# Kernel optimization log

Measured on AMD Instinct MI355X. Metric: run time of the kernel, lower is better.

The kernel has to match this reference:

```python
import jax, jax.numpy as jnp
import numpy as np

V = 50000   # words_num
D = 128     # embedding_dim
B = 2048    # batch
P = 20      # max Huffman path length


def setup_inputs() -> dict:
    key = jax.random.key(0)
    k1, k2, k3, k4, k5 = jax.random.split(key, 5)
    inputs_vector = jax.random.uniform(k1, (B, V), dtype=jnp.float32)
    path_nodes_indices = jax.random.randint(k2, (B, P), 0, V)
    huffman_codes = jax.random.randint(k3, (B, P), 0, 2).astype(jnp.float32)
    mask = jnp.ones((B, P), dtype=jnp.float32)
    # learned params, torch nn.Linear weight layout [out, in], kaiming-uniform-ish scale
    W_emb = jax.random.uniform(k4, (D, V), dtype=jnp.float32, minval=-1.0, maxval=1.0) / np.sqrt(V)
    W_cls = jax.random.uniform(k5, (V, D), dtype=jnp.float32, minval=-1.0, maxval=1.0) / np.sqrt(D)
    return {
        "inputs_vector": inputs_vector,
        "W_emb": W_emb,
        "W_cls": W_cls,
        "path_nodes_indices": path_nodes_indices,
        "huffman_codes": huffman_codes,
        "mask": mask,
    }


def _bce_with_logits(logits, targets):
    # numerically stable, elementwise (reduction='none')
    return jnp.maximum(logits, 0.0) - logits * targets + jnp.log1p(jnp.exp(-jnp.abs(logits)))


def reference(inputs_vector, W_emb, W_cls, path_nodes_indices, huffman_codes, mask):
    x = inputs_vector @ W_emb.T              # [B, D]  embedding Linear (no bias)
    logits_full = x @ W_cls.T                # [B, V]  full-vocab cls matmul (as in source)
    logits = jnp.take_along_axis(logits_full, path_nodes_indices, axis=1)  # [B, P]
    loss = _bce_with_logits(logits, huffman_codes)  # [B, P]
    masked_loss = loss * mask
    per_sample = masked_loss.sum(axis=-1) / mask.sum(axis=-1)  # [B]
    return per_sample.mean()
```

## Files before the change

kernel.cpp:

```cpp
#include <hip/hip_runtime.h>
#include <hip/hip_bf16.h>

#define V 50000
#define D 128
#define B 2048
#define P 20

#define BM 128
#define BK 64
#define NSPLIT 48
#define KC 1056
#define VPAD (NSPLIT * KC)
#define NSLICE (VPAD / 32)
#define NMT (B / BM)

typedef float  f32x4  __attribute__((ext_vector_type(4)));
typedef short  bf16x8 __attribute__((ext_vector_type(8)));
typedef unsigned int uint4v __attribute__((ext_vector_type(4)));

__device__ __forceinline__ unsigned int pk2(float a, float b) {
    return (__float_as_uint(b) & 0xFFFF0000u) | (__float_as_uint(a) >> 16);
}
__device__ __forceinline__ unsigned short f2bf(float f) {
    unsigned int u = __float_as_uint(f);
    return (unsigned short)((u + 0x7FFFu + ((u >> 16) & 1u)) >> 16);
}
__device__ __forceinline__ bf16x8 pack8(f32x4 lo, f32x4 hi) {
    union { uint4v u; bf16x8 h; } r;
    r.u.x = pk2(lo[0], lo[1]); r.u.y = pk2(lo[2], lo[3]);
    r.u.z = pk2(hi[0], hi[1]); r.u.w = pk2(hi[2], hi[3]);
    return r.h;
}

__global__ __launch_bounds__(256)
void w2v_wcast(const float* __restrict__ Wemb, unsigned short* __restrict__ WTF) {
    __shared__ unsigned short L[128 * 128];
    const int bk = blockIdx.x;
    const int t  = threadIdx.x;
    const int d = t >> 1, h = t & 1;
    const float* src = Wemb + (size_t)d * V + bk * 128 + h * 64;
#pragma unroll
    for (int j = 0; j < 8; ++j) {
        const int kg = bk * 128 + h * 64 + j * 8;
        f32x4 v0 = {0,0,0,0}, v1 = {0,0,0,0};
        if (kg + 8 <= V) {
            const f32x4* p = reinterpret_cast<const f32x4*>(src + j * 8);
            v0 = p[0]; v1 = p[1];
        }
        uint4v u;
        u.x = pk2(v0[0], v0[1]); u.y = pk2(v0[2], v0[3]);
        u.z = pk2(v1[0], v1[1]); u.w = pk2(v1[2], v1[3]);
        const int c8 = h * 8 + j;
        *reinterpret_cast<uint4v*>((char*)L + d * 256 + ((c8 ^ (d & 15)) << 4)) = u;
    }
    __syncthreads();
    const int w = t >> 6, l = t & 63;
    const int kg4 = l >> 4, fr = l & 15;
#pragma unroll
    for (int sl = 0; sl < 4; ++sl)
#pragma unroll
        for (int j2 = 0; j2 < 2; ++j2) {
            const int n  = w + j2 * 4;
            const int dd = n * 16 + fr;
            const int c8 = sl * 4 + kg4;
            uint4v u = *reinterpret_cast<const uint4v*>(
                (char*)L + dd * 256 + ((c8 ^ (dd & 15)) << 4));
            *reinterpret_cast<uint4v*>(
                (char*)WTF + ((size_t)(bk * 4 + sl) * 8 + n) * 1024 + l * 16) = u;
        }
}

template<int FAST>
__global__ __launch_bounds__(256, 3)
void w2v_gemm(const float* __restrict__ Ain, const void* __restrict__ Wsrc,
              void* __restrict__ part) {
    __shared__ unsigned short Sm[2 * BM * BK];
    char* AsB = (char*)Sm;
    char* WsB = (char*)(Sm + BM * BK);

    const int i   = blockIdx.x;
    const int xcd = i & 7;
    const int q   = i >> 3;
    const int s   = xcd * 6 + (q >> 4);
    const int mt  = q & 15;
    const int m0  = mt * BM;
    const int k0  = s * KC;
    const int k1  = (k0 + KC < V) ? (k0 + KC) : V;
    const int nsteps = (k1 - k0 + 63) >> 6;

    const int tid  = threadIdx.x;
    const int lane = tid & 63;
    const int wid  = tid >> 6;
    const int w32  = wid * 32;
    const int fr   = lane & 15;
    const int kg4  = lane >> 4;

    f32x4 acc[2][8] = {};

    const int rbase = tid >> 3;
    const int c8    = tid & 7;
    const int c8x   = c8 ^ (rbase & 7);
    const float* aBase = Ain + (size_t)(m0 + rbase) * V + c8 * 8;
    const unsigned short* WT = (const unsigned short*)Wsrc;
    const float*          Wf = (const float*)Wsrc;

    f32x4 aR[8];
    uint4v wR[4];
    f32x4 wRf[8];

    auto loadregs = [&](int ks) {
        const bool ag = (ks + c8 * 8 + 8 <= k1);
#pragma unroll
        for (int it = 0; it < 4; ++it) {
            const float* ap = aBase + (size_t)(it * 32) * V + ks;
            if (ag) {
                aR[it * 2]     = *reinterpret_cast<const f32x4*>(ap);
                aR[it * 2 + 1] = *reinterpret_cast<const f32x4*>(ap + 4);
            } else {
                aR[it * 2] = f32x4{0.f, 0.f, 0.f, 0.f};
                aR[it * 2 + 1] = f32x4{0.f, 0.f, 0.f, 0.f};
            }
        }
        if (FAST) {
            const char* wb = (const char*)WT + (size_t)(ks >> 5) * 8192 + tid * 16;
#pragma unroll
            for (int it = 0; it < 4; ++it)
                wR[it] = *reinterpret_cast<const uint4v*>(wb + it * 4096);
        } else {
            const bool wg = (ks + c8 * 8 + 8 <= V);
#pragma unroll
            for (int it = 0; it < 4; ++it) {
                const float* wp = Wf + (size_t)(rbase + it * 32) * V + c8 * 8 + ks;
                if (wg) {
                    wRf[it * 2]     = *reinterpret_cast<const f32x4*>(wp);
                    wRf[it * 2 + 1] = *reinterpret_cast<const f32x4*>(wp + 4);
                } else {
                    wRf[it * 2] = f32x4{0.f, 0.f, 0.f, 0.f};
                    wRf[it * 2 + 1] = f32x4{0.f, 0.f, 0.f, 0.f};
                }
            }
        }
    };

    auto writeLDS = [&]() {
#pragma unroll
        for (int it = 0; it < 4; ++it) {
            const unsigned dstA = (unsigned)((rbase + it * 32) * 128) + (unsigned)(c8x * 16);
            uint4v ua;
            ua.x = pk2(aR[it * 2][0], aR[it * 2][1]);
            ua.y = pk2(aR[it * 2][2], aR[it * 2][3]);
            ua.z = pk2(aR[it * 2 + 1][0], aR[it * 2 + 1][1]);
            ua.w = pk2(aR[it * 2 + 1][2], aR[it * 2 + 1][3]);
            *reinterpret_cast<uint4v*>(AsB + dstA) = ua;
            if (FAST) {
                *reinterpret_cast<uint4v*>(WsB + tid * 16 + it * 4096) = wR[it];
            } else {
                const int d = rbase + it * 32;
                const unsigned dstW = (unsigned)(((c8 >> 2) * 8 + (d >> 4)) * 1024
                                     + ((c8 & 3) * 16 + (d & 15)) * 16);
                uint4v uw;
                uw.x = pk2(wRf[it * 2][0], wRf[it * 2][1]);
                uw.y = pk2(wRf[it * 2][2], wRf[it * 2][3]);
                uw.z = pk2(wRf[it * 2 + 1][0], wRf[it * 2 + 1][1]);
                uw.w = pk2(wRf[it * 2 + 1][2], wRf[it * 2 + 1][3]);
                *reinterpret_cast<uint4v*>(WsB + dstW) = uw;
            }
        }
    };

    loadregs(k0);

    for (int t = 0; t < nsteps; ++t) {
        writeLDS();
        asm volatile("s_waitcnt lgkmcnt(0)" ::: "memory");
        __builtin_amdgcn_s_barrier();
        if (t + 1 < nsteps) loadregs(k0 + (t + 1) * 64);
#pragma unroll
        for (int kk = 0; kk < BK; kk += 32) {
            const int cbase = (kk >> 3) + kg4;
            bf16x8 af[2];
#pragma unroll
            for (int m = 0; m < 2; ++m) {
                const int r = w32 + m * 16 + fr;
                af[m] = *reinterpret_cast<const bf16x8*>(
                    AsB + r * 128 + ((cbase ^ (r & 7)) << 4));
            }
#pragma unroll
            for (int n = 0; n < 8; ++n) {
                const bf16x8 wf = *reinterpret_cast<const bf16x8*>(
                    WsB + ((kk >> 5) * 8 + n) * 1024 + lane * 16);
                acc[0][n] = __builtin_amdgcn_mfma_f32_16x16x32_bf16(af[0], wf, acc[0][n], 0, 0, 0);
                acc[1][n] = __builtin_amdgcn_mfma_f32_16x16x32_bf16(af[1], wf, acc[1][n], 0, 0, 0);
            }
        }
        asm volatile("s_waitcnt lgkmcnt(0)" ::: "memory");
        __builtin_amdgcn_s_barrier();
    }

    if (!FAST) {
        float* outp = (float*)part;
#pragma unroll
        for (int m = 0; m < 2; ++m) {
            const int r0 = m0 + w32 + m * 16 + kg4 * 4;
#pragma unroll
            for (int n = 0; n < 8; ++n) {
                const int c = n * 16 + fr;
#pragma unroll
                for (int jj = 0; jj < 4; ++jj)
                    atomicAdd(&outp[(size_t)(r0 + jj) * D + c], acc[m][n][jj]);
            }
        }
        return;
    }
    unsigned short* Cs = Sm;
#pragma unroll
    for (int m = 0; m < 2; ++m) {
        const int r0 = w32 + m * 16 + kg4 * 4;
#pragma unroll
        for (int n = 0; n < 8; ++n) {
            const int c = n * 16 + fr;
#pragma unroll
            for (int jj = 0; jj < 4; ++jj)
                Cs[(r0 + jj) * 128 + c] = f2bf(acc[m][n][jj]);
        }
    }
    __syncthreads();
    char* dstb = (char*)part + ((size_t)s * B + m0) * (D * 2);
#pragma unroll
    for (int it = 0; it < 8; ++it) {
        const int off = (it * 256 + tid) * 16;
        uint4v v = *reinterpret_cast<const uint4v*>((char*)Sm + off);
        *reinterpret_cast<uint4v*>(dstb + off) = v;
    }
}

__global__ __launch_bounds__(256)
void w2v_loss(const void* __restrict__ part, int part_bf16,
              const float* __restrict__ Wcls, const int* __restrict__ pathIdx,
              const float* __restrict__ codes, const float* __restrict__ mask,
              float* __restrict__ out) {
    const int lane = threadIdx.x & 63;
    const int wid  = threadIdx.x >> 6;
    const int b    = blockIdx.x * 4 + wid;

    float x0 = 0.f, x1 = 0.f;
    if (part_bf16) {
        const unsigned* pb = (const unsigned*)part;
#pragma unroll 8
        for (int s = 0; s < NSPLIT; ++s) {
            unsigned u = pb[((size_t)s * B + b) * 64 + lane];
            x0 += __uint_as_float(u << 16);
            x1 += __uint_as_float(u & 0xFFFF0000u);
        }
    } else {
        const float* pf = (const float*)part;
        const float2 v = *reinterpret_cast<const float2*>(&pf[(size_t)b * D + lane * 2]);
        x0 = v.x; x1 = v.y;
    }

    float lsum = 0.f, msum = 0.f;
#pragma unroll
    for (int p = 0; p < P; ++p) {
        int node = pathIdx[b * P + p];
        const float2 w = *reinterpret_cast<const float2*>(&Wcls[(size_t)node * D + lane * 2]);
        float d = x0 * w.x + x1 * w.y;
#pragma unroll
        for (int off = 1; off < 64; off <<= 1)
            d += __shfl_xor(d, off, 64);
        float t  = codes[b * P + p];
        float mm = mask[b * P + p];
        float loss = fmaxf(d, 0.f) - d * t + log1pf(__expf(-fabsf(d)));
        lsum += loss * mm;
        msum += mm;
    }
    float per = (msum > 0.f) ? (lsum / msum) : 0.f;

    __shared__ float wsum[4];
    if (lane == 0) wsum[wid] = per;
    __syncthreads();
    if (threadIdx.x == 0) {
        float ssum = wsum[0] + wsum[1] + wsum[2] + wsum[3];
        atomicAdd(out, ssum * (1.0f / (float)B));
    }
}

extern "C" void kernel_launch(void* const* d_in, const int* in_sizes, int n_in,
                              void* d_out, int out_size, void* d_ws, size_t ws_size,
                              hipStream_t stream) {
    const float* inputs = (const float*)d_in[0];
    const float* W_emb  = (const float*)d_in[1];
    const float* W_cls  = (const float*)d_in[2];
    const int*   path   = (const int*)  d_in[3];
    const float* codes  = (const float*)d_in[4];
    const float* mask   = (const float*)d_in[5];
    float* out = (float*)d_out;

    hipMemsetAsync(d_out, 0, sizeof(float), stream);

    const size_t wtf_bytes  = (size_t)NSLICE * 8192;
    const size_t part_off   = (wtf_bytes + 255) & ~(size_t)255;
    const size_t part_bytes = (size_t)NSPLIT * B * D * 2;

    if (ws_size >= part_off + part_bytes) {
        unsigned short* WTF = (unsigned short*)d_ws;
        char* partp = (char*)d_ws + part_off;
        w2v_wcast<<<dim3(VPAD / 128), dim3(256), 0, stream>>>(W_emb, WTF);
        w2v_gemm<1><<<dim3(NMT * NSPLIT), dim3(256), 0, stream>>>(inputs, WTF, partp);
        w2v_loss<<<dim3(B / 4), dim3(256), 0, stream>>>(partp, 1, W_cls, path, codes, mask, out);
    } else {
        hipMemsetAsync(d_ws, 0, (size_t)B * D * sizeof(float), stream);
        w2v_gemm<0><<<dim3(NMT * NSPLIT), dim3(256), 0, stream>>>(inputs, W_emb, d_ws);
        w2v_loss<<<dim3(B / 4), dim3(256), 0, stream>>>(d_ws, 0, W_cls, path, codes, mask, out);
    }
}
```

Before: 142.6 us.

## Retile embedding GEMM to BM=32 with fewer K-splits and double-buffered LDS

Shrinks the M tile from 128 to 32 rows and reduces the split-K count from 48 to 16, so each block covers a longer K range (49 steps) with a 32x128 output tile split across four waves. LDS becomes double-buffered for A and W, the A layout changes to match the MFMA fragment order, and occupancy is raised to 4 blocks/CU. This is meant to cut the partial-sum traffic written and then reduced in the loss kernel and to improve latency hiding. The cost is that each block re-reads its W slice for only 32 rows, so W traffic rises fourfold, and per-block MFMA work per barrier is lower.

```diff
diff --git a/kernel.cpp b/kernel.cpp
--- a/kernel.cpp
+++ b/kernel.cpp
@@ -6,10 +6,11 @@
 #define B 2048
 #define P 20
 
-#define BM 128
+#define BM 32
 #define BK 64
-#define NSPLIT 48
-#define KC 1056
+#define NSPLIT 16
+#define KC 3136
+#define NSTEPS 49
 #define VPAD (NSPLIT * KC)
 #define NSLICE (VPAD / 32)
 #define NMT (B / BM)
@@ -71,166 +72,162 @@
 }
 
 template<int FAST>
-__global__ __launch_bounds__(256, 3)
+__global__ __launch_bounds__(256, 4)
 void w2v_gemm(const float* __restrict__ Ain, const void* __restrict__ Wsrc,
               void* __restrict__ part) {
-    __shared__ unsigned short Sm[2 * BM * BK];
-    char* AsB = (char*)Sm;
-    char* WsB = (char*)(Sm + BM * BK);
+    __shared__ char smem[40960];
 
     const int i   = blockIdx.x;
     const int xcd = i & 7;
-    const int q   = i >> 3;
-    const int s   = xcd * 6 + (q >> 4);
-    const int mt  = q & 15;
+    const int j   = i >> 3;
+    const int s   = xcd * 2 + (j >> 6);
+    const int mt  = j & 63;
     const int m0  = mt * BM;
     const int k0  = s * KC;
-    const int k1  = (k0 + KC < V) ? (k0 + KC) : V;
-    const int nsteps = (k1 - k0 + 63) >> 6;
 
     const int tid  = threadIdx.x;
     const int lane = tid & 63;
     const int wid  = tid >> 6;
-    const int w32  = wid * 32;
     const int fr   = lane & 15;
     const int kg4  = lane >> 4;
 
-    f32x4 acc[2][8] = {};
-
-    const int rbase = tid >> 3;
-    const int c8    = tid & 7;
-    const int c8x   = c8 ^ (rbase & 7);
-    const float* aBase = Ain + (size_t)(m0 + rbase) * V + c8 * 8;
+    f32x4 acc[2][2] = {};
+
+    const int arow = tid >> 3;
+    const int c8   = tid & 7;
+    const float* aSrc = Ain + (size_t)(m0 + arow) * V + c8 * 8;
+    const unsigned dstA = (unsigned)(((c8 >> 2) * 2 + (arow >> 4)) * 1024
+                          + ((c8 & 3) * 16 + (arow & 15)) * 16);
+
     const unsigned short* WT = (const unsigned short*)Wsrc;
     const float*          Wf = (const float*)Wsrc;
 
-    f32x4 aR[8];
+    f32x4 aR[2];
     uint4v wR[4];
-    f32x4 wRf[8];
 
     auto loadregs = [&](int ks) {
-        const bool ag = (ks + c8 * 8 + 8 <= k1);
-#pragma unroll
-        for (int it = 0; it < 4; ++it) {
-            const float* ap = aBase + (size_t)(it * 32) * V + ks;
-            if (ag) {
-                aR[it * 2]     = *reinterpret_cast<const f32x4*>(ap);
-                aR[it * 2 + 1] = *reinterpret_cast<const f32x4*>(ap + 4);
-            } else {
-                aR[it * 2] = f32x4{0.f, 0.f, 0.f, 0.f};
-                aR[it * 2 + 1] = f32x4{0.f, 0.f, 0.f, 0.f};
-            }
+        const int kg = ks + c8 * 8;
+        if (kg + 8 <= V) {
+            const f32x4* ap = reinterpret_cast<const f32x4*>(aSrc + ks);
+            aR[0] = ap[0]; aR[1] = ap[1];
+        } else {
+            aR[0] = f32x4{0.f, 0.f, 0.f, 0.f};
+            aR[1] = f32x4{0.f, 0.f, 0.f, 0.f};
         }
         if (FAST) {
             const char* wb = (const char*)WT + (size_t)(ks >> 5) * 8192 + tid * 16;
 #pragma unroll
             for (int it = 0; it < 4; ++it)
                 wR[it] = *reinterpret_cast<const uint4v*>(wb + it * 4096);
-        } else {
-            const bool wg = (ks + c8 * 8 + 8 <= V);
-#pragma unroll
-            for (int it = 0; it < 4; ++it) {
-                const float* wp = Wf + (size_t)(rbase + it * 32) * V + c8 * 8 + ks;
-                if (wg) {
-                    wRf[it * 2]     = *reinterpret_cast<const f32x4*>(wp);
-                    wRf[it * 2 + 1] = *reinterpret_cast<const f32x4*>(wp + 4);
-                } else {
-                    wRf[it * 2] = f32x4{0.f, 0.f, 0.f, 0.f};
-                    wRf[it * 2 + 1] = f32x4{0.f, 0.f, 0.f, 0.f};
+        }
+    };
+    auto writeLDS = [&](int cur) {
+        uint4v ua;
+        ua.x = pk2(aR[0][0], aR[0][1]); ua.y = pk2(aR[0][2], aR[0][3]);
+        ua.z = pk2(aR[1][0], aR[1][1]); ua.w = pk2(aR[1][2], aR[1][3]);
+        *reinterpret_cast<uint4v*>(smem + cur * 4096 + dstA) = ua;
+        if (FAST) {
+#pragma unroll
+            for (int it = 0; it < 4; ++it)
+                *reinterpret_cast<uint4v*>(smem + 8192 + cur * 16384 + tid * 16 + it * 4096) = wR[it];
+        }
+    };
+
+    if (FAST) {
+        loadregs(k0);
+        for (int t = 0; t < NSTEPS; ++t) {
+            const int cur = t & 1;
+            writeLDS(cur);
+            asm volatile("s_waitcnt lgkmcnt(0)" ::: "memory");
+            __builtin_amdgcn_s_barrier();
+            if (t + 1 < NSTEPS) loadregs(k0 + (t + 1) * 64);
+            const char* Ab = smem + cur * 4096;
+            const char* Wb2 = smem + 8192 + cur * 16384;
+#pragma unroll
+            for (int kc = 0; kc < 2; ++kc) {
+                bf16x8 af[2];
+#pragma unroll
+                for (int mf = 0; mf < 2; ++mf)
+                    af[mf] = *reinterpret_cast<const bf16x8*>(
+                        Ab + (kc * 2 + mf) * 1024 + lane * 16);
+#pragma unroll
+                for (int nn = 0; nn < 2; ++nn) {
+                    const bf16x8 wf = *reinterpret_cast<const bf16x8*>(
+                        Wb2 + (kc * 8 + wid * 2 + nn) * 1024 + lane * 16);
+                    acc[0][nn] = __builtin_amdgcn_mfma_f32_16x16x32_bf16(af[0], wf, acc[0][nn], 0, 0, 0);
+                    acc[1][nn] = __builtin_amdgcn_mfma_f32_16x16x32_bf16(af[1], wf, acc[1][nn], 0, 0, 0);
                 }
             }
-        }
-    };
-
-    auto writeLDS = [&]() {
-#pragma unroll
-        for (int it = 0; it < 4; ++it) {
-            const unsigned dstA = (unsigned)((rbase + it * 32) * 128) + (unsigned)(c8x * 16);
-            uint4v ua;
-            ua.x = pk2(aR[it * 2][0], aR[it * 2][1]);
-            ua.y = pk2(aR[it * 2][2], aR[it * 2][3]);
-            ua.z = pk2(aR[it * 2 + 1][0], aR[it * 2 + 1][1]);
-            ua.w = pk2(aR[it * 2 + 1][2], aR[it * 2 + 1][3]);
-            *reinterpret_cast<uint4v*>(AsB + dstA) = ua;
-            if (FAST) {
-                *reinterpret_cast<uint4v*>(WsB + tid * 16 + it * 4096) = wR[it];
-            } else {
-                const int d = rbase + it * 32;
-                const unsigned dstW = (unsigned)(((c8 >> 2) * 8 + (d >> 4)) * 1024
-                                     + ((c8 & 3) * 16 + (d & 15)) * 16);
-                uint4v uw;
-                uw.x = pk2(wRf[it * 2][0], wRf[it * 2][1]);
-                uw.y = pk2(wRf[it * 2][2], wRf[it * 2][3]);
-                uw.z = pk2(wRf[it * 2 + 1][0], wRf[it * 2 + 1][1]);
-                uw.w = pk2(wRf[it * 2 + 1][2], wRf[it * 2 + 1][3]);
-                *reinterpret_cast<uint4v*>(WsB + dstW) = uw;
+            asm volatile("s_waitcnt lgkmcnt(0)" ::: "memory");
+            __builtin_amdgcn_s_barrier();
+        }
+    } else {
+        for (int t = 0; t < NSTEPS; ++t) {
+            const int ks = k0 + t * 64;
+            loadregs(ks);
+            writeLDS(0);
+            __syncthreads();
+#pragma unroll
+            for (int kc = 0; kc < 2; ++kc) {
+                bf16x8 af[2];
+#pragma unroll
+                for (int mf = 0; mf < 2; ++mf)
+                    af[mf] = *reinterpret_cast<const bf16x8*>(
+                        smem + (kc * 2 + mf) * 1024 + lane * 16);
+#pragma unroll
+                for (int nn = 0; nn < 2; ++nn) {
+                    const int dd = (wid * 2 + nn) * 16 + fr;
+                    const int kg = ks + kc * 32 + kg4 * 8;
+                    f32x4 lo = {0,0,0,0}, hi = {0,0,0,0};
+                    if (kg + 8 <= V) {
+                        const f32x4* p = reinterpret_cast<const f32x4*>(Wf + (size_t)dd * V + kg);
+                        lo = p[0]; hi = p[1];
+                    }
+                    const bf16x8 wf = pack8(lo, hi);
+                    acc[0][nn] = __builtin_amdgcn_mfma_f32_16x16x32_bf16(af[0], wf, acc[0][nn], 0, 0, 0);
+                    acc[1][nn] = __builtin_amdgcn_mfma_f32_16x16x32_bf16(af[1], wf, acc[1][nn], 0, 0, 0);
+                }
             }
-        }
-    };
-
-    loadregs(k0);
-
-    for (int t = 0; t < nsteps; ++t) {
-        writeLDS();
-        asm volatile("s_waitcnt lgkmcnt(0)" ::: "memory");
-        __builtin_amdgcn_s_barrier();
-        if (t + 1 < nsteps) loadregs(k0 + (t + 1) * 64);
-#pragma unroll
-        for (int kk = 0; kk < BK; kk += 32) {
-            const int cbase = (kk >> 3) + kg4;
-            bf16x8 af[2];
-#pragma unroll
-            for (int m = 0; m < 2; ++m) {
-                const int r = w32 + m * 16 + fr;
-                af[m] = *reinterpret_cast<const bf16x8*>(
-                    AsB + r * 128 + ((cbase ^ (r & 7)) << 4));
-            }
-#pragma unroll
-            for (int n = 0; n < 8; ++n) {
-                const bf16x8 wf = *reinterpret_cast<const bf16x8*>(
-                    WsB + ((kk >> 5) * 8 + n) * 1024 + lane * 16);
-                acc[0][n] = __builtin_amdgcn_mfma_f32_16x16x32_bf16(af[0], wf, acc[0][n], 0, 0, 0);
-                acc[1][n] = __builtin_amdgcn_mfma_f32_16x16x32_bf16(af[1], wf, acc[1][n], 0, 0, 0);
-            }
-        }
-        asm volatile("s_waitcnt lgkmcnt(0)" ::: "memory");
-        __builtin_amdgcn_s_barrier();
+            __syncthreads();
+        }
     }
 
     if (!FAST) {
         float* outp = (float*)part;
 #pragma unroll
-        for (int m = 0; m < 2; ++m) {
-            const int r0 = m0 + w32 + m * 16 + kg4 * 4;
-#pragma unroll
-            for (int n = 0; n < 8; ++n) {
-                const int c = n * 16 + fr;
+        for (int mf = 0; mf < 2; ++mf) {
+            const int r0 = m0 + mf * 16 + kg4 * 4;
+#pragma unroll
+            for (int nn = 0; nn < 2; ++nn) {
+                const int c = (wid * 2 + nn) * 16 + fr;
 #pragma unroll
                 for (int jj = 0; jj < 4; ++jj)
-                    atomicAdd(&outp[(size_t)(r0 + jj) * D + c], acc[m][n][jj]);
+                    atomicAdd(&outp[(size_t)(r0 + jj) * D + c], acc[mf][nn][jj]);
             }
         }
         return;
     }
-    unsigned short* Cs = Sm;
-#pragma unroll
-    for (int m = 0; m < 2; ++m) {
-        const int r0 = w32 + m * 16 + kg4 * 4;
-#pragma unroll
-        for (int n = 0; n < 8; ++n) {
-            const int c = n * 16 + fr;
+    asm volatile("s_waitcnt lgkmcnt(0)" ::: "memory");
+    __builtin_amdgcn_s_barrier();
+    unsigned short* Cs = (unsigned short*)smem;
+#pragma unroll
+    for (int mf = 0; mf < 2; ++mf) {
+        const int r0 = mf * 16 + kg4 * 4;
+#pragma unroll
+        for (int nn = 0; nn < 2; ++nn) {
+            const int c = (wid * 2 + nn) * 16 + fr;
 #pragma unroll
             for (int jj = 0; jj < 4; ++jj)
-                Cs[(r0 + jj) * 128 + c] = f2bf(acc[m][n][jj]);
+                Cs[(r0 + jj) * 128 + c] = f2bf(acc[mf][nn][jj]);
         }
     }
     __syncthreads();
     char* dstb = (char*)part + ((size_t)s * B + m0) * (D * 2);
 #pragma unroll
-    for (int it = 0; it < 8; ++it) {
+    for (int it = 0; it < 2; ++it) {
         const int off = (it * 256 + tid) * 16;
-        uint4v v = *reinterpret_cast<const uint4v*>((char*)Sm + off);
-        *reinterpret_cast<uint4v*>(dstb + off) = v;
+        *reinterpret_cast<uint4v*>(dstb + off) =
+            *reinterpret_cast<const uint4v*>(smem + off);
     }
 }
 
@@ -246,7 +243,7 @@
     float x0 = 0.f, x1 = 0.f;
     if (part_bf16) {
         const unsigned* pb = (const unsigned*)part;
-#pragma unroll 8
+#pragma unroll
         for (int s = 0; s < NSPLIT; ++s) {
             unsigned u = pb[((size_t)s * B + b) * 64 + lane];
             x0 += __uint_as_float(u << 16);
```

Result: slower. 159.3 us (+11.8%).
